# Kernel optimization log

Measured on AMD Instinct MI355X. Metric: run time of the kernel, lower is better.

Reference implementation:

```python
import jax, jax.numpy as jnp
import numpy as np

B = 32          # graphs per batch
NPG = 2048      # nodes per graph
N = B * NPG     # 65536 total nodes
EPG = 16384     # edges per graph
E = B * EPG     # 524288 total edges
F_IN = 129
H, C = 4, 64    # heads, per-head channels
HC = H * C      # 256
NEG_SLOPE = 0.2 # GATConv LeakyReLU slope


def setup_inputs() -> dict:
    key = jax.random.key(0)
    ks = jax.random.split(key, 20)
    # node features
    x = jax.random.normal(ks[0], (N, F_IN), dtype=jnp.float32)
    # random edges, endpoints within the same graph (per-graph contiguous node ids)
    off = (jnp.arange(B) * NPG)[:, None]
    src = (jax.random.randint(ks[1], (B, EPG), 0, NPG) + off).reshape(-1)
    dst = (jax.random.randint(ks[2], (B, EPG), 0, NPG) + off).reshape(-1)
    edge_index = jnp.stack([src, dst]).astype(jnp.int64)

    def lin(k, fan_in, shape):
        return jax.random.normal(k, shape, dtype=jnp.float32) / np.sqrt(fan_in)

    return {
        "x": x,
        "edge_index": edge_index,
        "lin0_w": lin(ks[3], F_IN, (F_IN, 256)),
        "lin0_b": jnp.zeros((256,), jnp.float32),
        "gat0_W": lin(ks[4], 256, (256, HC)),
        "gat0_asrc": lin(ks[5], C, (H, C)),
        "gat0_adst": lin(ks[6], C, (H, C)),
        "gat0_b": jnp.zeros((HC,), jnp.float32),
        "pool0_w": lin(ks[7], HC, (HC,)),
        "gat1_W": lin(ks[8], HC, (HC, HC)),
        "gat1_asrc": lin(ks[9], C, (H, C)),
        "gat1_adst": lin(ks[10], C, (H, C)),
        "gat1_b": jnp.zeros((HC,), jnp.float32),
        "pool1_w": lin(ks[11], HC, (HC,)),
        "gate_w": lin(ks[12], HC, (HC, 1)),
        "gate_b": jnp.zeros((1,), jnp.float32),
    }


def _leaky(z):
    return jnp.where(z > 0, z, NEG_SLOPE * z)


def _gat(h_in, src, dst, emask, W, asrc, adst, b):
    """PyG GATConv: shared lin, edge attention, segment softmax over dest, self-loops, concat heads."""
    n = h_in.shape[0]
    h = (h_in @ W).reshape(n, H, C)                       # [n,H,C]
    loops = jnp.arange(n)
    s = jnp.concatenate([src, loops])                     # add self loops
    d = jnp.concatenate([dst, loops])
    m = jnp.concatenate([emask, jnp.ones((n,), bool)])
    a_s = jnp.einsum('nhc,hc->nh', h, asrc)               # [n,H]
    a_d = jnp.einsum('nhc,hc->nh', h, adst)
    logit = _leaky(a_s[s] + a_d[d])                       # [E+n,H]
    logit = jnp.where(m[:, None], logit, -1e9)
    mx = jax.ops.segment_max(logit, d, num_segments=n)    # stable segment softmax
    ex = jnp.exp(logit - mx[d]) * m[:, None].astype(logit.dtype)
    den = jax.ops.segment_sum(ex, d, num_segments=n)
    coef = ex / (den[d] + 1e-16)                          # [E+n,H]
    out = jax.ops.segment_sum(h[s] * coef[:, :, None], d, num_segments=n)
    return out.reshape(n, HC) + b


def _topk_pool(hx, src, dst, emask, w, n_in, k):
    """PyG TopKPooling: score = x.w/||w||, per-graph top-k, x' = x[perm]*tanh(score[perm]), edge filter+reindex."""
    n_tot = hx.shape[0]
    bb = n_tot // n_in
    score = (hx @ w) / (jnp.linalg.norm(w) + 1e-16)       # [n_tot]
    _, idx = jax.lax.top_k(score.reshape(bb, n_in), k)    # [bb,k]
    perm = (idx + (jnp.arange(bb) * n_in)[:, None]).reshape(-1)
    xs = hx[perm] * jnp.tanh(score[perm])[:, None]
    newid = jnp.full((n_tot,), -1, jnp.int32).at[perm].set(jnp.arange(bb * k, dtype=jnp.int32))
    ns, nd = newid[src], newid[dst]
    valid = emask & (ns >= 0) & (nd >= 0)
    ns = jnp.where(valid, ns, 0)
    nd = jnp.where(valid, nd, 0)
    return xs, ns, nd, valid


def _attpool(hx, n, gate_w, gate_b):
    """AttentionalAggregation: softmax(gate_nn(x)) per graph, weighted sum."""
    bb = hx.shape[0] // n
    gate = (hx @ gate_w + gate_b).reshape(bb, n)
    wts = jax.nn.softmax(gate, axis=1)
    return jnp.einsum('bn,bnf->bf', wts, hx.reshape(bb, n, -1))


def reference(x, edge_index, lin0_w, lin0_b, gat0_W, gat0_asrc, gat0_adst, gat0_b,
              pool0_w, gat1_W, gat1_asrc, gat1_adst, gat1_b, pool1_w, gate_w, gate_b):
    src, dst = edge_index[0], edge_index[1]
    emask = jnp.ones((E,), bool)
    h = jax.nn.relu(x @ lin0_w + lin0_b)                                  # hidden MLP
    h = jax.nn.elu(_gat(h, src, dst, emask, gat0_W, gat0_asrc, gat0_adst, gat0_b))
    h, src, dst, emask = _topk_pool(h, src, dst, emask, pool0_w, NPG, NPG // 2)
    out = _attpool(h, NPG // 2, gate_w, gate_b)                           # [B,256]
    h = jax.nn.elu(_gat(h, src, dst, emask, gat1_W, gat1_asrc, gat1_adst, gat1_b))
    h, src, dst, emask = _topk_pool(h, src, dst, emask, pool1_w, NPG // 2, NPG // 4)
    out = out + _attpool(h, NPG // 4, gate_w, gate_b)
    return out
```

## Files before the change

kernel.cpp:

```cpp
#include <hip/hip_runtime.h>
#include <cmath>

namespace {

constexpr int NN0 = 65536;
constexpr int NB  = 32;
constexpr int NE  = 524288;
constexpr int EPG = 16384;
constexpr int FIN = 129;
constexpr int KP  = 160;

typedef short bf16x8 __attribute__((ext_vector_type(8)));
typedef float f32x4 __attribute__((ext_vector_type(4)));

__device__ inline float leakyrelu(float z) { return z > 0.f ? z : 0.2f * z; }
__device__ inline float eluf(float z) { return z > 0.f ? z : __expf(z) - 1.f; }
__device__ inline float ftanh(float z) {
  float t = __expf(2.f * z);
  return (t - 1.f) / (t + 1.f);
}

__device__ inline unsigned short f2bf(float x) {
  union { float f; unsigned int u; } v; v.f = x;
  unsigned int r = v.u + 0x7fffu + ((v.u >> 16) & 1u);
  return (unsigned short)(r >> 16);
}
__device__ inline float bf2f(unsigned short h) {
  union { unsigned int u; float f; } v; v.u = ((unsigned int)h) << 16;
  return v.f;
}

__device__ inline float4 f4fma(float4 a, float c, float4 acc) {
  acc.x += a.x * c; acc.y += a.y * c; acc.z += a.z * c; acc.w += a.w * c;
  return acc;
}

__device__ inline int swz_block(int bid, int bpgl) {
  int x = bid & 7;
  int local = bid >> 3;
  int g = x + ((local >> bpgl) << 3);
  return (g << bpgl) + (local & ((1 << bpgl) - 1));
}

__device__ __forceinline__ void gload_lds16(const unsigned short* g, unsigned short* l) {
  __builtin_amdgcn_global_load_lds((const unsigned int*)g, (unsigned int*)l, 16, 0, 0);
}

__device__ inline void pack_w_body(const float* __restrict__ W, int Kreal, int idx,
                                   unsigned short* __restrict__ hi,
                                   unsigned short* __restrict__ lo) {
  int j = idx & 7;
  int lane = (idx >> 3) & 63;
  int ct = (idx >> 9) & 15;
  int kt = idx >> 13;
  int k = kt * 32 + ((lane >> 4) << 3) + j;
  int c = ct * 16 + (lane & 15);
  float v = (k < Kreal) ? W[(size_t)k * 256 + c] : 0.f;
  unsigned short h = f2bf(v);
  hi[idx] = h;
  lo[idx] = f2bf(v - bf2f(h));
}

constexpr int SLC = 8;

__global__ __launch_bounds__(1024) void prep(
    const float* __restrict__ x,
    const float* __restrict__ w0, const float* __restrict__ w1,
    const float* __restrict__ w2,
    const float* __restrict__ pw0, const float* __restrict__ pw1,
    const int* __restrict__ src, const int* __restrict__ dst,
    unsigned short* __restrict__ xhi, unsigned short* __restrict__ xlo,
    unsigned short* __restrict__ whi0, unsigned short* __restrict__ wlo0,
    unsigned short* __restrict__ whi1, unsigned short* __restrict__ wlo1,
    unsigned short* __restrict__ whi2, unsigned short* __restrict__ wlo2,
    float* __restrict__ norms, int* __restrict__ newid,
    int* __restrict__ cursor, int* __restrict__ csr) {
  __shared__ int cnt[2048];
  __shared__ int basev[2048];
  const int NSC = NB * SLC;
  const int NX = NN0 * KP / 8192;
  const int NW0 = 5 * 8192 / 1024;
  const int NW = 8 * 8192 / 1024;
  const int NC = NN0 / 1024;
  int b = blockIdx.x, tid = threadIdx.x;
  if (b < NSC) {
    const int g = b / SLC, sl = b % SLC;
    const int e0 = g * EPG + sl * (EPG / SLC);
    const int ne = EPG / SLC;
    cnt[tid] = 0; cnt[tid + 1024] = 0;
    __syncthreads();
    for (int i = tid; i < ne; i += 1024)
      atomicAdd(&cnt[dst[e0 + i] - (g << 11)], 1);
    __syncthreads();
    for (int k = tid; k < 2048; k += 1024) {
      int c = cnt[k];
      basev[k] = c ? atomicAdd(&cursor[(g << 11) + k], c) : 0;
    }
    __syncthreads();
    cnt[tid] = 0; cnt[tid + 1024] = 0;
    __syncthreads();
    for (int i = tid; i < ne; i += 1024) {
      int e = e0 + i;
      int d = dst[e];
      int lb = d - (g << 11);
      int pos = basev[lb] + atomicAdd(&cnt[lb], 1);
      if (pos < 64) csr[(size_t)d * 64 + pos] = src[e];
    }
    return;
  }
  b -= NSC;
  if (b < NX) {
    const int base = (b * 1024 + tid) * 8;
    const int row = base / KP;
    const int c0 = base - row * KP;
    const float* xr = &x[(size_t)row * FIN];
    bf16x8 hv, lv;
#pragma unroll
    for (int i = 0; i < 8; i++) {
      const int c = c0 + i;
      float v = (c < FIN) ? xr[c] : 0.f;
      unsigned short h = f2bf(v);
      hv[i] = (short)h;
      lv[i] = (short)f2bf(v - bf2f(h));
    }
    *reinterpret_cast<bf16x8*>(&xhi[base]) = hv;
    *reinterpret_cast<bf16x8*>(&xlo[base]) = lv;
    return;
  }
  b -= NX;
  if (b < NW0) { pack_w_body(w0, FIN, b * 1024 + tid, whi0, wlo0); return; }
  b -= NW0;
  if (b < NW) { pack_w_body(w1, 256, b * 1024 + tid, whi1, wlo1); return; }
  b -= NW;
  if (b < NW) { pack_w_body(w2, 256, b * 1024 + tid, whi2, wlo2); return; }
  b -= NW;
  if (b < NC) {
    newid[b * 1024 + tid] = -1;
    return;
  }
  if (tid < 64) {
    float a0 = 0.f, a1 = 0.f;
#pragma unroll
    for (int j = tid; j < 256; j += 64) {
      float v0 = pw0[j]; a0 += v0 * v0;
      float v1 = pw1[j]; a1 += v1 * v1;
    }
#pragma unroll
    for (int off = 32; off >= 1; off >>= 1) {
      a0 += __shfl_xor(a0, off);
      a1 += __shfl_xor(a1, off);
    }
    if (tid == 0) {
      norms[0] = 1.f / (sqrtf(a0) + 1e-16f);
      norms[1] = 1.f / (sqrtf(a1) + 1e-16f);
    }
  }
}

__global__ __launch_bounds__(256, 2) void gemm_fused(
    const unsigned short* __restrict__ Xhi, const unsigned short* __restrict__ Xlo,
    const unsigned short* __restrict__ B0hi, const unsigned short* __restrict__ B0lo,
    const float* __restrict__ bias0,
    const unsigned short* __restrict__ B1hi, const unsigned short* __restrict__ B1lo,
    float* __restrict__ Out,
    const float* __restrict__ attsrc, const float* __restrict__ attdst,
    float* __restrict__ a_s, float* __restrict__ a_d) {
  __shared__ __align__(16) unsigned short As[2][2][64][32];
  __shared__ __align__(16) char Hsh[2][64 * 512];
  const int tid = threadIdx.x;
  const int lane = tid & 63;
  const int w = tid >> 6;
  const int row0 = blockIdx.x * 64;
  const int l15 = lane & 15, q = lane >> 4;
  const int srow16 = lane >> 2;
  const int skc = (lane & 3) * 8;

  auto stage = [&](int nb, int kt) {
    const size_t goff = (size_t)(row0 + w * 16 + srow16) * KP + kt * 32 + skc;
    gload_lds16(Xhi + goff, &As[nb][0][w * 16][0]);
    gload_lds16(Xlo + goff, &As[nb][1][w * 16][0]);
  };

  f32x4 acc[4][4];
#pragma unroll
  for (int mf = 0; mf < 4; mf++)
#pragma unroll
    for (int nf = 0; nf < 4; nf++) acc[mf][nf] = (f32x4)(0.f);

  stage(0, 0);
  __syncthreads();

#pragma unroll
  for (int kt = 0; kt < 5; ++kt) {
    const int nb = kt & 1;
    if (kt + 1 < 5) stage(nb ^ 1, kt + 1);
    bf16x8 bh[4], bl[4];
#pragma unroll
    for (int nf = 0; nf < 4; nf++) {
      const int ct = w * 4 + nf;
      const size_t bbase = ((size_t)((kt * 16 + ct) * 64 + lane)) << 3;
      bh[nf] = *reinterpret_cast<const bf16x8*>(B0hi + bbase);
      bl[nf] = *reinterpret_cast<const bf16x8*>(B0lo + bbase);
    }
#pragma unroll
    for (int mf = 0; mf < 4; mf++) {
      const int ar = mf * 16 + l15;
      bf16x8 ah = *reinterpret_cast<const bf16x8*>(&As[nb][0][ar][q * 8]);
      bf16x8 al = *reinterpret_cast<const bf16x8*>(&As[nb][1][ar][q * 8]);
#pragma unroll
      for (int nf = 0; nf < 4; nf++) {
        acc[mf][nf] = __builtin_amdgcn_mfma_f32_16x16x32_bf16(ah, bh[nf], acc[mf][nf], 0, 0, 0);
        acc[mf][nf] = __builtin_amdgcn_mfma_f32_16x16x32_bf16(ah, bl[nf], acc[mf][nf], 0, 0, 0);
        acc[mf][nf] = __builtin_amdgcn_mfma_f32_16x16x32_bf16(al, bh[nf], acc[mf][nf], 0, 0, 0);
      }
    }
    __syncthreads();
  }

#pragma unroll
  for (int mf = 0; mf < 4; mf++) {
#pragma unroll
    for (int r = 0; r < 4; r++) {
      const int row = mf * 16 + q * 4 + r;
#pragma unroll
      for (int nf = 0; nf < 4; nf++) {
        const int col = w * 64 + nf * 16 + l15;
        float v = acc[mf][nf][r] + bias0[col];
        v = fmaxf(v, 0.f);
        unsigned short h = f2bf(v);
        unsigned short l = f2bf(v - bf2f(h));
        unsigned int off = (unsigned int)(row * 512 + col * 2) ^ ((row & 7) << 4);
        *reinterpret_cast<unsigned short*>(&Hsh[0][off]) = h;
        *reinterpret_cast<unsigned short*>(&Hsh[1][off]) = l;
        acc[mf][nf][r] = 0.f;
      }
    }
  }
  __syncthreads();

#pragma unroll
  for (int kt = 0; kt < 8; ++kt) {
    bf16x8 bh[4], bl[4];
#pragma unroll
    for (int nf = 0; nf < 4; nf++) {
      const int ct = w * 4 + nf;
      const size_t bbase = ((size_t)((kt * 16 + ct) * 64 + lane)) << 3;
      bh[nf] = *reinterpret_cast<const bf16x8*>(B1hi + bbase);
      bl[nf] = *reinterpret_cast<const bf16x8*>(B1lo + bbase);
    }
#pragma unroll
    for (int mf = 0; mf < 4; mf++) {
      const int ar = mf * 16 + l15;
      unsigned int off = (unsigned int)(ar * 512 + kt * 64 + q * 16) ^ ((ar & 7) << 4);
      bf16x8 ah = *reinterpret_cast<const bf16x8*>(&Hsh[0][off]);
      bf16x8 al = *reinterpret_cast<const bf16x8*>(&Hsh[1][off]);
#pragma unroll
      for (int nf = 0; nf < 4; nf++) {
        acc[mf][nf] = __builtin_amdgcn_mfma_f32_16x16x32_bf16(ah, bh[nf], acc[mf][nf], 0, 0, 0);
        acc[mf][nf] = __builtin_amdgcn_mfma_f32_16x16x32_bf16(ah, bl[nf], acc[mf][nf], 0, 0, 0);
        acc[mf][nf] = __builtin_amdgcn_mfma_f32_16x16x32_bf16(al, bh[nf], acc[mf][nf], 0, 0, 0);
      }
    }
  }

#pragma unroll
  for (int mf = 0; mf < 4; mf++) {
    const int rowb = row0 + mf * 16 + q * 4;
#pragma unroll
    for (int r = 0; r < 4; r++) {
#pragma unroll
      for (int nf = 0; nf < 4; nf++) {
        const int col = w * 64 + nf * 16 + l15;
        Out[(size_t)(rowb + r) * 256 + col] = acc[mf][nf][r];
      }
    }
  }
  const int head = w;
  float sv[4], dv[4];
#pragma unroll
  for (int nf = 0; nf < 4; nf++) {
    sv[nf] = attsrc[head * 64 + nf * 16 + l15];
    dv[nf] = attdst[head * 64 + nf * 16 + l15];
  }
#pragma unroll
  for (int mf = 0; mf < 4; mf++) {
#pragma unroll
    for (int r = 0; r < 4; r++) {
      float ps = 0.f, pd = 0.f;
#pragma unroll
      for (int nf = 0; nf < 4; nf++) {
        ps += acc[mf][nf][r] * sv[nf];
        pd += acc[mf][nf][r] * dv[nf];
      }
#pragma unroll
      for (int off = 8; off >= 1; off >>= 1) {
        ps += __shfl_xor(ps, off);
        pd += __shfl_xor(pd, off);
      }
      if (l15 == 0) {
        const int row = row0 + mf * 16 + q * 4 + r;
        a_s[(size_t)row * 4 + head] = ps;
        a_d[(size_t)row * 4 + head] = pd;
      }
    }
  }
}

template <int KT, bool INDIR>
__global__ __launch_bounds__(256, 2) void gemm_mfma(
    const unsigned short* __restrict__ Xhi, const unsigned short* __restrict__ Xlo,
    int ldx,
    const unsigned short* __restrict__ Bhi, const unsigned short* __restrict__ Blo,
    float* __restrict__ Out,
    const float* __restrict__ attsrc, const float* __restrict__ attdst,
    float* __restrict__ a_s, float* __restrict__ a_d,
    const int* __restrict__ rowmap, const float* __restrict__ tscale, int swzl,
    int ngemm, const float* __restrict__ partials, float* __restrict__ outp,
    int nch) {
  __shared__ __align__(16) unsigned short As[2][2][128][32];
  const int tid = threadIdx.x;
  if ((int)blockIdx.x >= ngemm) {
    int g = blockIdx.x - ngemm, c = tid;
    float a = 0.f;
    for (int s = 0; s < nch; s++) a += partials[((size_t)g * nch + s) * 256 + c];
    outp[g * 256 + c] = a;
    return;
  }
  const int lane = tid & 63;
  const int w = tid >> 6;
  const int rb = (swzl >= 0) ? swz_block(blockIdx.x, swzl) : blockIdx.x;
  const int row0 = rb * 128;
  const int l15 = lane & 15, q = lane >> 4;
  const int sl4 = lane >> 2;
  const int skc = (lane & 3) * 8;

  size_t gr[2];
#pragma unroll
  for (int i = 0; i < 2; i++) {
    int lr = row0 + (w + 4 * i) * 16 + sl4;
    gr[i] = INDIR ? (size_t)rowmap[lr] : (size_t)lr;
  }

  auto stage = [&](int nb, int kt) {
#pragma unroll
    for (int i = 0; i < 2; i++) {
      const int rbase = (w + 4 * i) * 16;
      const size_t goff = gr[i] * ldx + kt * 32 + skc;
      gload_lds16(Xhi + goff, &As[nb][0][rbase][0]);
      gload_lds16(Xlo + goff, &As[nb][1][rbase][0]);
    }
  };

  f32x4 acc[8][4];
#pragma unroll
  for (int mf = 0; mf < 8; mf++)
#pragma unroll
    for (int nf = 0; nf < 4; nf++) acc[mf][nf] = (f32x4)(0.f);

  stage(0, 0);
  __syncthreads();

#pragma unroll
  for (int kt = 0; kt < KT; ++kt) {
    const int nb = kt & 1;
    if (kt + 1 < KT) stage(nb ^ 1, kt + 1);
    bf16x8 bh[4], bl[4];
#pragma unroll
    for (int nf = 0; nf < 4; nf++) {
      const int ct = w * 4 + nf;
      const size_t bbase = ((size_t)((kt * 16 + ct) * 64 + lane)) << 3;
      bh[nf] = *reinterpret_cast<const bf16x8*>(Bhi + bbase);
      bl[nf] = *reinterpret_cast<const bf16x8*>(Blo + bbase);
    }
#pragma unroll
    for (int mf = 0; mf < 8; mf++) {
      const int ar = mf * 16 + l15;
      bf16x8 ah = *reinterpret_cast<const bf16x8*>(&As[nb][0][ar][q * 8]);
      bf16x8 al = *reinterpret_cast<const bf16x8*>(&As[nb][1][ar][q * 8]);
#pragma unroll
      for (int nf = 0; nf < 4; nf++) {
        acc[mf][nf] = __builtin_amdgcn_mfma_f32_16x16x32_bf16(ah, bh[nf], acc[mf][nf], 0, 0, 0);
        acc[mf][nf] = __builtin_amdgcn_mfma_f32_16x16x32_bf16(ah, bl[nf], acc[mf][nf], 0, 0, 0);
        acc[mf][nf] = __builtin_amdgcn_mfma_f32_16x16x32_bf16(al, bh[nf], acc[mf][nf], 0, 0, 0);
      }
    }
    __syncthreads();
  }

#pragma unroll
  for (int mf = 0; mf < 8; mf++) {
    const int rowb = row0 + mf * 16 + q * 4;
#pragma unroll
    for (int r = 0; r < 4; r++) {
      const float ts = INDIR ? tscale[rowb + r] : 1.f;
#pragma unroll
      for (int nf = 0; nf < 4; nf++) {
        float v = acc[mf][nf][r];
        if constexpr (INDIR) v *= ts;
        const int col = w * 64 + nf * 16 + l15;
        Out[(size_t)(rowb + r) * 256 + col] = v;
      }
    }
  }
  const int head = w;
  float sv[4], dv[4];
#pragma unroll
  for (int nf = 0; nf < 4; nf++) {
    sv[nf] = attsrc[head * 64 + nf * 16 + l15];
    dv[nf] = attdst[head * 64 + nf * 16 + l15];
  }
#pragma unroll
  for (int mf = 0; mf < 8; mf++) {
#pragma unroll
    for (int r = 0; r < 4; r++) {
      float ps = 0.f, pd = 0.f;
#pragma unroll
      for (int nf = 0; nf < 4; nf++) {
        ps += acc[mf][nf][r] * sv[nf];
        pd += acc[mf][nf][r] * dv[nf];
      }
#pragma unroll
      for (int off = 8; off >= 1; off >>= 1) {
        ps += __shfl_xor(ps, off);
        pd += __shfl_xor(pd, off);
      }
      if (l15 == 0) {
        const int row = row0 + mf * 16 + q * 4 + r;
        float ts = INDIR ? tscale[row] : 1.f;
        a_s[(size_t)row * 4 + head] = ps * ts;
        a_d[(size_t)row * 4 + head] = pd * ts;
      }
    }
  }
}

__global__ __launch_bounds__(256) void gat_node8(
    const int* __restrict__ cursor, const int* __restrict__ csr,
    const float* __restrict__ a_s, const float* __restrict__ a_d,
    const float* __restrict__ hW, const float* __restrict__ bias,
    const float* __restrict__ pool_w, const float* __restrict__ inv_norm,
    const float* __restrict__ gate_w,
    unsigned short* __restrict__ outHi, unsigned short* __restrict__ outLo,
    float* __restrict__ score, float* __restrict__ graw, int bpgl) {
  const int lane = threadIdx.x & 63;
  const int wv = threadIdx.x >> 6;
  const int dbase = swz_block(blockIdx.x, bpgl) * 8 + wv * 2;
  const int g = lane >> 4, l16 = lane & 15;
  const int d = dbase + (g >> 1);
  const int h0 = (g & 1) * 2;

  const int deg = min(cursor[d], 63);
  const int dim = deg + 1;

  int dmaxw = dim;
  dmaxw = max(dmaxw, __shfl_xor(dmaxw, 32));
  const int nch = (dmaxw + 15) >> 4;

  const float2 ad2 = *reinterpret_cast<const float2*>(&a_d[(size_t)d * 4 + h0]);

  int sreg[4];
  float L0[4], L1[4];
#pragma unroll
  for (int c = 0; c < 4; c++) {
    if (c < nch) {
      const int j = c * 16 + l16;
      const bool has = j < dim;
      int s = (j < deg) ? csr[(size_t)d * 64 + j] : d;
      sreg[c] = s;
      float2 as2 = *reinterpret_cast<const float2*>(&a_s[(size_t)s * 4 + h0]);
      L0[c] = has ? leakyrelu(as2.x + ad2.x) : -1e30f;
      L1[c] = has ? leakyrelu(as2.y + ad2.y) : -1e30f;
    } else {
      sreg[c] = d;
      L0[c] = -1e30f; L1[c] = -1e30f;
    }
  }
  float m0 = fmaxf(fmaxf(L0[0], L0[1]), fmaxf(L0[2], L0[3]));
  float m1 = fmaxf(fmaxf(L1[0], L1[1]), fmaxf(L1[2], L1[3]));
#pragma unroll
  for (int off = 1; off <= 8; off <<= 1) {
    m0 = fmaxf(m0, __shfl_xor(m0, off));
    m1 = fmaxf(m1, __shfl_xor(m1, off));
  }
  float e0[4], e1[4];
  float dn0 = 0.f, dn1 = 0.f;
#pragma unroll
  for (int c = 0; c < 4; c++) {
    if (c < nch) {
      e0[c] = __expf(L0[c] - m0);
      e1[c] = __expf(L1[c] - m1);
      dn0 += e0[c]; dn1 += e1[c];
    } else {
      e0[c] = 0.f; e1[c] = 0.f;
    }
  }
#pragma unroll
  for (int off = 1; off <= 8; off <<= 1) {
    dn0 += __shfl_xor(dn0, off);
    dn1 += __shfl_xor(dn1, off);
  }

  float4 acc0 = {0.f, 0.f, 0.f, 0.f}, acc1 = {0.f, 0.f, 0.f, 0.f};
#pragma unroll
  for (int c = 0; c < 4; c++) {
    if (c < nch) {
      const int tmax = min(16, dmaxw - c * 16);
#pragma unroll 4
      for (int tt = 0; tt < tmax; tt++) {
        const int idx = g * 16 + tt;
        int st = __shfl(sreg[c], idx);
        float c0 = __shfl(e0[c], idx), c1 = __shfl(e1[c], idx);
        if (c * 16 + tt < dim) {
          const float4* hp = reinterpret_cast<const float4*>(&hW[(size_t)st * 256]) + l16;
          acc0 = f4fma(hp[h0 * 16],       c0, acc0);
          acc1 = f4fma(hp[(h0 + 1) * 16], c1, acc1);
        }
      }
    }
  }

  const float iv0 = 1.f / (dn0 + 1e-16f), iv1 = 1.f / (dn1 + 1e-16f);
  float sd = 0.f, gd = 0.f;
#pragma unroll
  for (int h = 0; h < 2; h++) {
    const int coff = (h0 + h) * 64 + l16 * 4;
    float4 vb = h ? acc1 : acc0;
    float iv = h ? iv1 : iv0;
    float4 bb = *reinterpret_cast<const float4*>(&bias[coff]);
    float4 o;
    o.x = eluf(vb.x * iv + bb.x);
    o.y = eluf(vb.y * iv + bb.y);
    o.z = eluf(vb.z * iv + bb.z);
    o.w = eluf(vb.w * iv + bb.w);
    ushort4 oh, ol;
    oh.x = f2bf(o.x); ol.x = f2bf(o.x - bf2f(oh.x));
    oh.y = f2bf(o.y); ol.y = f2bf(o.y - bf2f(oh.y));
    oh.z = f2bf(o.z); ol.z = f2bf(o.z - bf2f(oh.z));
    oh.w = f2bf(o.w); ol.w = f2bf(o.w - bf2f(oh.w));
    *reinterpret_cast<ushort4*>(&outHi[(size_t)d * 256 + coff]) = oh;
    *reinterpret_cast<ushort4*>(&outLo[(size_t)d * 256 + coff]) = ol;
    float4 pw = *reinterpret_cast<const float4*>(&pool_w[coff]);
    float4 gw = *reinterpret_cast<const float4*>(&gate_w[coff]);
    sd += o.x * pw.x + o.y * pw.y + o.z * pw.z + o.w * pw.w;
    gd += o.x * gw.x + o.y * gw.y + o.z * gw.z + o.w * gw.w;
  }
#pragma unroll
  for (int off = 1; off <= 16; off <<= 1) {
    sd += __shfl_xor(sd, off);
    gd += __shfl_xor(gd, off);
  }
  if ((lane & 31) == 0) {
    score[d] = sd * inv_norm[0];
    graw[d] = gd;
  }
}

__global__ __launch_bounds__(1024) void topk_hsel(
    const float* __restrict__ score, const float* __restrict__ graw,
    const float* __restrict__ gate_b, int npg, int k,
    int* __restrict__ perm, int* __restrict__ newid,
    float* __restrict__ gate, float* __restrict__ tsc) {
  __shared__ unsigned keys[2048];
  __shared__ int hist[1024];
  __shared__ int ssum[1024];
  __shared__ int segtot[16];
  __shared__ unsigned wmin[16], wmax[16];
  __shared__ int sstate[3];
  __shared__ int scnt;
  __shared__ int candi[512];
  __shared__ unsigned candk[512];
  __shared__ float fred[1024];
  const int g = blockIdx.x, tid = threadIdx.x;
  const int wv = tid >> 6, ln = tid & 63;
  const size_t base = (size_t)g * npg;

  unsigned mymin = 0xFFFFFFFFu, mymax = 0u;
  for (int i = tid; i < npg; i += 1024) {
    unsigned u = __float_as_uint(score[base + i]);
    u = (u & 0x80000000u) ? ~u : (u | 0x80000000u);
    keys[i] = u;
    mymin = min(mymin, u);
    mymax = max(mymax, u);
  }
#pragma unroll
  for (int off = 32; off >= 1; off >>= 1) {
    mymin = min(mymin, (unsigned)__shfl_xor((int)mymin, off));
    mymax = max(mymax, (unsigned)__shfl_xor((int)mymax, off));
  }
  if (ln == 0) { wmin[wv] = mymin; wmax[wv] = mymax; }
  __syncthreads();
  unsigned lo, hi;
  {
    unsigned a = 0xFFFFFFFFu, b = 0u;
#pragma unroll
    for (int i = 0; i < 16; i++) { a = min(a, wmin[i]); b = max(b, wmax[i]); }
    lo = a; hi = b;
  }
  int need = k;

  for (int iter = 0; iter < 4; ++iter) {
    unsigned long long range = (unsigned long long)(hi - lo) + 1ull;
    unsigned width = (unsigned)((range + 1023ull) >> 10);
    hist[tid] = 0;
    __syncthreads();
    for (int i = tid; i < npg; i += 1024) {
      unsigned u = keys[i];
      if (u >= lo && u <= hi) atomicAdd(&hist[(u - lo) / width], 1);
    }
    __syncthreads();
    int v = hist[tid];
    int s = v;
#pragma unroll
    for (int off = 1; off < 64; off <<= 1) {
      int t = __shfl_down(s, off);
      if (ln + off < 64) s += t;
    }
    if (ln == 0) segtot[wv] = s;
    __syncthreads();
    if (tid == 0) {
      int acc = 0;
      for (int i = 15; i >= 0; i--) { int t = segtot[i]; segtot[i] = acc; acc += t; }
    }
    __syncthreads();
    int S = s + segtot[wv];
    ssum[tid] = S;
    __syncthreads();
    int gt = (tid == 1023) ? 0 : ssum[tid + 1];
    if (S >= need && gt < need) {
      sstate[0] = tid;
      sstate[1] = gt;
      sstate[2] = hist[tid];
    }
    __syncthreads();
    const int bstar = sstate[0], cntAbove = sstate[1], m = sstate[2];
    unsigned nlo = lo + (unsigned)bstar * width;
    unsigned long long nhiu = (unsigned long long)lo + (unsigned long long)(bstar + 1) * width - 1ull;
    unsigned nhi = (nhiu > (unsigned long long)hi) ? hi : (unsigned)nhiu;
    need -= cntAbove;
    lo = nlo; hi = nhi;
    __syncthreads();
    if (width == 1 || m <= 256) break;
  }

  if (tid == 0) scnt = 0;
  __syncthreads();
  for (int i = tid; i < npg; i += 1024) {
    unsigned u = keys[i];
    if (u >= lo && u <= hi) {
      int pidx = atomicAdd(&scnt, 1);
      if (pidx < 512) { candi[pidx] = i; candk[pidx] = u; }
    }
  }
  __syncthreads();
  const int m_all = scnt;
  const float gb = gate_b[0];
  if (tid == 0) scnt = 0;
  __syncthreads();
  for (int i = tid; i < npg; i += 1024) {
    if (keys[i] > hi) {
      int pos = atomicAdd(&scnt, 1);
      int node = (int)(base + i);
      perm[g * k + pos] = node;
      if (newid) newid[node] = g * k + pos;
      float ts = ftanh(score[base + i]);
      tsc[g * k + pos] = ts;
      gate[g * k + pos] = ts * graw[node] + gb;
    }
  }
  __syncthreads();
  const int nAbove = scnt;
  if (m_all <= 512) {
    for (int c = tid; c < m_all; c += 1024) {
      unsigned u = candk[c];
      int i = candi[c];
      int rank = 0;
      for (int j = 0; j < m_all; j++) {
        unsigned vk = candk[j];
        rank += (vk > u) || (vk == u && candi[j] < i);
      }
      if (rank < need) {
        int pos = nAbove + rank;
        int node = (int)(base + i);
        perm[g * k + pos] = node;
        if (newid) newid[node] = g * k + pos;
        float ts = ftanh(score[base + i]);
        tsc[g * k + pos] = ts;
        gate[g * k + pos] = ts * graw[node] + gb;
      }
    }
  } else {
    for (int i = tid; i < npg; i += 1024) {
      unsigned u = keys[i];
      if (u >= lo && u <= hi) {
        int rank = 0;
        for (int j = 0; j < npg; j++) {
          unsigned vk = keys[j];
          if (vk >= lo && vk <= hi) rank += (vk > u) || (vk == u && j < i);
        }
        if (rank < need) {
          int pos = nAbove + rank;
          int node = (int)(base + i);
          perm[g * k + pos] = node;
          if (newid) newid[node] = g * k + pos;
          float ts = ftanh(score[base + i]);
          tsc[g * k + pos] = ts;
          gate[g * k + pos] = ts * graw[node] + gb;
        }
      }
    }
  }
  __syncthreads();

  float gv = (tid < k) ? gate[g * k + tid] : -1e30f;
  fred[tid] = gv;
  __syncthreads();
  for (int s = 512; s >= 1; s >>= 1) {
    if (tid < s) fred[tid] = fmaxf(fred[tid], fred[tid + s]);
    __syncthreads();
  }
  const float gm = fred[0];
  __syncthreads();
  float ge = (tid < k) ? __expf(gv - gm) : 0.f;
  fred[tid] = ge;
  __syncthreads();
  for (int s = 512; s >= 1; s >>= 1) {
    if (tid < s) fred[tid] += fred[tid + s];
    __syncthreads();
  }
  const float ginv = 1.f / fred[0];
  if (tid < k) gate[g * k + tid] = ge * ginv * tsc[g * k + tid];
}

__global__ __launch_bounds__(1024) void pool_tail(
    const unsigned short* __restrict__ xhi, const unsigned short* __restrict__ xlo,
    const int* __restrict__ perm, const float* __restrict__ wfin,
    float* __restrict__ partials, int npg, int bpgl, int nsc,
    const int* __restrict__ src, const int* __restrict__ dst,
    const int* __restrict__ newid, int* __restrict__ cursor2,
    int* __restrict__ csr) {
  __shared__ int cnt[1024];
  __shared__ int basev[1024];
  const int tid = threadIdx.x;
  if ((int)blockIdx.x < nsc) {
    const int g = blockIdx.x / SLC, sl = blockIdx.x % SLC;
    const int e0 = g * EPG + sl * (EPG / SLC);
    const int ne = EPG / SLC;
    cnt[tid] = 0;
    __syncthreads();
    for (int i = tid; i < ne; i += 1024) {
      int e = e0 + i;
      int s = newid[src[e]], d = newid[dst[e]];
      if (s >= 0 && d >= 0) atomicAdd(&cnt[d - (g << 10)], 1);
    }
    __syncthreads();
    {
      int c = cnt[tid];
      basev[tid] = c ? atomicAdd(&cursor2[(g << 10) + tid], c) : 0;
    }
    __syncthreads();
    cnt[tid] = 0;
    __syncthreads();
    for (int i = tid; i < ne; i += 1024) {
      int e = e0 + i;
      int s = newid[src[e]], d = newid[dst[e]];
      if (s < 0 || d < 0) continue;
      int lb = d - (g << 10);
      int pos = basev[lb] + atomicAdd(&cnt[lb], 1);
      if (pos < 64) csr[(size_t)d * 64 + pos] = s;
    }
    return;
  }
  int rel = blockIdx.x - nsc;
  int o = swz_block(rel, bpgl);
  int g = o >> bpgl, lb = o & ((1 << bpgl) - 1);
  int part = tid >> 8, c = tid & 255;
  int sub = lb * 4 + part;
  size_t r0 = (size_t)g * npg + sub * 32;
  float a = 0.f;
#pragma unroll 8
  for (int i = 0; i < 32; i++) {
    float wv = wfin[r0 + i];
    size_t node = (size_t)perm[r0 + i];
    float v = bf2f(xhi[node * 256 + c]) + bf2f(xlo[node * 256 + c]);
    a += wv * v;
  }
  partials[((size_t)g * (npg >> 5) + sub) * 256 + c] = a;
}

__global__ __launch_bounds__(256) void attpool_reduce(const float* __restrict__ partials,
                                                      float* __restrict__ out,
                                                      int nch, int acc_flag) {
  int g = blockIdx.x, c = threadIdx.x;
  float a = 0.f;
  for (int s = 0; s < nch; s++) a += partials[((size_t)g * nch + s) * 256 + c];
  if (acc_flag) out[g * 256 + c] += a;
  else out[g * 256 + c] = a;
}

}

extern "C" void kernel_launch(void* const* d_in, const int* in_sizes, int n_in,
                              void* d_out, int out_size, void* d_ws, size_t ws_size,
                              hipStream_t stream) {
  (void)in_sizes; (void)n_in; (void)out_size; (void)ws_size;
  const float* x       = (const float*)d_in[0];
  const int*   ei      = (const int*)d_in[1];
  const float* lin0_w  = (const float*)d_in[2];
  const float* lin0_b  = (const float*)d_in[3];
  const float* gat0_W  = (const float*)d_in[4];
  const float* gat0_as = (const float*)d_in[5];
  const float* gat0_ad = (const float*)d_in[6];
  const float* gat0_b  = (const float*)d_in[7];
  const float* pool0_w = (const float*)d_in[8];
  const float* gat1_W  = (const float*)d_in[9];
  const float* gat1_as = (const float*)d_in[10];
  const float* gat1_ad = (const float*)d_in[11];
  const float* gat1_b  = (const float*)d_in[12];
  const float* pool1_w = (const float*)d_in[13];
  const float* gate_w  = (const float*)d_in[14];
  const float* gate_b  = (const float*)d_in[15];
  float* out = (float*)d_out;
  const int* srcp = ei;
  const int* dstp = ei + NE;

  char* wsb = (char*)d_ws;
  size_t cur = 0;
  auto alloc = [&](size_t bytes) {
    void* p = wsb + cur;
    cur = (cur + bytes + 255) & ~(size_t)255;
    return p;
  };
  char* regA = (char*)alloc((size_t)NN0 * 256 * 4);
  char* regB = (char*)alloc((size_t)NN0 * 256 * 4);
  char* regD = (char*)alloc((size_t)NN0 * KP * 2 * 2);
  float* a_s     = (float*)alloc((size_t)NN0 * 4 * 4);
  float* a_d     = (float*)alloc((size_t)NN0 * 4 * 4);
  int*   cursor  = (int*)alloc((size_t)NN0 * 4);
  int*   cursor2 = (int*)alloc((size_t)32768 * 4);
  int*   csr     = (int*)alloc((size_t)NN0 * 64 * 4);
  float* score   = (float*)alloc((size_t)NN0 * 4);
  float* graw    = (float*)alloc((size_t)NN0 * 4);
  int*   newid   = (int*)alloc((size_t)NN0 * 4);
  int*   perm0   = (int*)alloc((size_t)32768 * 4);
  int*   perm1   = (int*)alloc((size_t)16384 * 4);
  float* tsc0    = (float*)alloc((size_t)32768 * 4);
  float* tsc1    = (float*)alloc((size_t)16384 * 4);
  float* gate0   = (float*)alloc((size_t)32768 * 4);
  float* gate1   = (float*)alloc((size_t)16384 * 4);
  float* partials= (float*)alloc((size_t)NB * 32 * 256 * 4);
  float* norms   = (float*)alloc(2 * 4);
  unsigned short* whi0 = (unsigned short*)alloc((size_t)5 * 8192 * 2);
  unsigned short* wlo0 = (unsigned short*)alloc((size_t)5 * 8192 * 2);
  unsigned short* whi1 = (unsigned short*)alloc((size_t)8 * 8192 * 2);
  unsigned short* wlo1 = (unsigned short*)alloc((size_t)8 * 8192 * 2);
  unsigned short* whi2 = (unsigned short*)alloc((size_t)8 * 8192 * 2);
  unsigned short* wlo2 = (unsigned short*)alloc((size_t)8 * 8192 * 2);

  unsigned short* xhi = (unsigned short*)regD;
  unsigned short* xlo = xhi + (size_t)NN0 * KP;
  float* hW0  = (float*)regB;
  unsigned short* out0hi = (unsigned short*)regA;
  unsigned short* out0lo = out0hi + (size_t)NN0 * 256;
  float* hW1  = (float*)regB;
  unsigned short* out1hi = (unsigned short*)(regB + (size_t)32768 * 256 * 4);
  unsigned short* out1lo = out1hi + (size_t)32768 * 256;

  hipMemsetAsync(cursor, 0, (size_t)NN0 * 4, stream);
  hipMemsetAsync(cursor2, 0, (size_t)32768 * 4, stream);

  {
    int grid = NB * SLC + NN0 * KP / 8192 + 40 + 64 + 64 + 64 + 1;
    prep<<<grid, 1024, 0, stream>>>(x, lin0_w, gat0_W, gat1_W, pool0_w, pool1_w,
                                    srcp, dstp,
                                    xhi, xlo, whi0, wlo0, whi1, wlo1, whi2, wlo2,
                                    norms, newid, cursor, csr);
  }

  gemm_fused<<<NN0 / 64, 256, 0, stream>>>(
      xhi, xlo, whi0, wlo0, lin0_b, whi1, wlo1, hW0,
      gat0_as, gat0_ad, a_s, a_d);

  gat_node8<<<NN0 / 8, 256, 0, stream>>>(cursor, csr, a_s, a_d, hW0,
                                         gat0_b, pool0_w, norms, gate_w,
                                         out0hi, out0lo, score, graw, 8);

  topk_hsel<<<NB, 1024, 0, stream>>>(score, graw, gate_b, 2048, 1024,
                                     perm0, newid, gate0, tsc0);
  pool_tail<<<NB * SLC + NB * 8, 1024, 0, stream>>>(
      out0hi, out0lo, perm0, gate0, partials, 1024, 3, NB * SLC,
      srcp, dstp, newid, cursor2, csr);

  gemm_mfma<8, true><<<32768 / 128 + NB, 256, 0, stream>>>(
      out0hi, out0lo, 256, whi2, wlo2, hW1,
      gat1_as, gat1_ad, a_s, a_d, perm0, tsc0, 3,
      32768 / 128, partials, out, 32);

  gat_node8<<<32768 / 8, 256, 0, stream>>>(cursor2, csr, a_s, a_d, hW1,
                                           gat1_b, pool1_w, norms + 1, gate_w,
                                           out1hi, out1lo, score, graw, 7);

  topk_hsel<<<NB, 1024, 0, stream>>>(score, graw, gate_b, 1024, 512,
                                     perm1, nullptr, gate1, tsc1);
  pool_tail<<<NB * 4, 1024, 0, stream>>>(
      out1hi, out1lo, perm1, gate1, partials, 512, 2, 0,
      nullptr, nullptr, nullptr, nullptr, nullptr);
  attpool_reduce<<<NB, 256, 0, stream>>>(partials, out, 16, 1);
}
```

Measured before the change: 249.3 us.

## Halve intermediate LDS buffer in fused GEMM by staging second GEMM in two K halves

The fused two-GEMM kernel now keeps the ReLU'd first-GEMM output packed as bf16 hi/lo pairs in registers. It writes only half of the K dimension to shared memory at a time: waves 0-1 write, everyone runs four K-steps, then waves 2-3 write and the rest runs. This halves the Hsh LDS buffer and raises launch bounds to 3 blocks per CU to increase occupancy. In exchange it adds two extra block barriers and 64 packed registers per thread, which may cause spills under the tighter register budget.

```diff
diff --git a/kernel.cpp b/kernel.cpp
--- a/kernel.cpp
+++ b/kernel.cpp
@@ -157,7 +157,7 @@
   }
 }
 
-__global__ __launch_bounds__(256, 2) void gemm_fused(
+__global__ __launch_bounds__(256, 3) void gemm_fused(
     const unsigned short* __restrict__ Xhi, const unsigned short* __restrict__ Xlo,
     const unsigned short* __restrict__ B0hi, const unsigned short* __restrict__ B0lo,
     const float* __restrict__ bias0,
@@ -166,7 +166,7 @@
     const float* __restrict__ attsrc, const float* __restrict__ attdst,
     float* __restrict__ a_s, float* __restrict__ a_d) {
   __shared__ __align__(16) unsigned short As[2][2][64][32];
-  __shared__ __align__(16) char Hsh[2][64 * 512];
+  __shared__ __align__(16) char Hsh[2][64 * 256];
   const int tid = threadIdx.x;
   const int lane = tid & 63;
   const int w = tid >> 6;
@@ -217,51 +217,87 @@
     __syncthreads();
   }
 
+  unsigned hp[32], lp[32];
 #pragma unroll
   for (int mf = 0; mf < 4; mf++) {
 #pragma unroll
-    for (int r = 0; r < 4; r++) {
-      const int row = mf * 16 + q * 4 + r;
+    for (int nf = 0; nf < 4; nf++) {
+      const int col = w * 64 + nf * 16 + l15;
+      const float bb = bias0[col];
+#pragma unroll
+      for (int rp = 0; rp < 2; rp++) {
+        float v0 = fmaxf(acc[mf][nf][2 * rp] + bb, 0.f);
+        float v1 = fmaxf(acc[mf][nf][2 * rp + 1] + bb, 0.f);
+        unsigned short h0 = f2bf(v0);
+        unsigned short l0 = f2bf(v0 - bf2f(h0));
+        unsigned short h1 = f2bf(v1);
+        unsigned short l1 = f2bf(v1 - bf2f(h1));
+        const int i = mf * 8 + nf * 2 + rp;
+        hp[i] = (unsigned)h0 | ((unsigned)h1 << 16);
+        lp[i] = (unsigned)l0 | ((unsigned)l1 << 16);
+        acc[mf][nf][2 * rp] = 0.f;
+        acc[mf][nf][2 * rp + 1] = 0.f;
+      }
+    }
+  }
+
+  auto writeHalf = [&]() {
+#pragma unroll
+    for (int mf = 0; mf < 4; mf++) {
 #pragma unroll
       for (int nf = 0; nf < 4; nf++) {
-        const int col = w * 64 + nf * 16 + l15;
-        float v = acc[mf][nf][r] + bias0[col];
-        v = fmaxf(v, 0.f);
-        unsigned short h = f2bf(v);
-        unsigned short l = f2bf(v - bf2f(h));
-        unsigned int off = (unsigned int)(row * 512 + col * 2) ^ ((row & 7) << 4);
-        *reinterpret_cast<unsigned short*>(&Hsh[0][off]) = h;
-        *reinterpret_cast<unsigned short*>(&Hsh[1][off]) = l;
-        acc[mf][nf][r] = 0.f;
-      }
-    }
-  }
-  __syncthreads();
-
-#pragma unroll
-  for (int kt = 0; kt < 8; ++kt) {
-    bf16x8 bh[4], bl[4];
-#pragma unroll
-    for (int nf = 0; nf < 4; nf++) {
-      const int ct = w * 4 + nf;
-      const size_t bbase = ((size_t)((kt * 16 + ct) * 64 + lane)) << 3;
-      bh[nf] = *reinterpret_cast<const bf16x8*>(B1hi + bbase);
-      bl[nf] = *reinterpret_cast<const bf16x8*>(B1lo + bbase);
-    }
-#pragma unroll
-    for (int mf = 0; mf < 4; mf++) {
-      const int ar = mf * 16 + l15;
-      unsigned int off = (unsigned int)(ar * 512 + kt * 64 + q * 16) ^ ((ar & 7) << 4);
-      bf16x8 ah = *reinterpret_cast<const bf16x8*>(&Hsh[0][off]);
-      bf16x8 al = *reinterpret_cast<const bf16x8*>(&Hsh[1][off]);
+#pragma unroll
+        for (int r = 0; r < 4; r++) {
+          const int i = mf * 8 + nf * 2 + (r >> 1);
+          unsigned short pv = (r & 1) ? (unsigned short)(hp[i] >> 16)
+                                      : (unsigned short)(hp[i] & 0xffffu);
+          unsigned short pl = (r & 1) ? (unsigned short)(lp[i] >> 16)
+                                      : (unsigned short)(lp[i] & 0xffffu);
+          const int row = mf * 16 + q * 4 + r;
+          const int colL = (w & 1) * 64 + nf * 16 + l15;
+          unsigned off = (unsigned)(row * 256 + colL * 2) ^ ((row & 7) << 4);
+          *reinterpret_cast<unsigned short*>(&Hsh[0][off]) = pv;
+          *reinterpret_cast<unsigned short*>(&Hsh[1][off]) = pl;
+        }
+      }
+    }
+  };
+
+  auto mfma4 = [&](int ktbase) {
+#pragma unroll
+    for (int ktp = 0; ktp < 4; ++ktp) {
+      const int kt = ktbase + ktp;
+      bf16x8 bh[4], bl[4];
 #pragma unroll
       for (int nf = 0; nf < 4; nf++) {
-        acc[mf][nf] = __builtin_amdgcn_mfma_f32_16x16x32_bf16(ah, bh[nf], acc[mf][nf], 0, 0, 0);
-        acc[mf][nf] = __builtin_amdgcn_mfma_f32_16x16x32_bf16(ah, bl[nf], acc[mf][nf], 0, 0, 0);
-        acc[mf][nf] = __builtin_amdgcn_mfma_f32_16x16x32_bf16(al, bh[nf], acc[mf][nf], 0, 0, 0);
-      }
-    }
-  }
+        const int ct = w * 4 + nf;
+        const size_t bbase = ((size_t)((kt * 16 + ct) * 64 + lane)) << 3;
+        bh[nf] = *reinterpret_cast<const bf16x8*>(B1hi + bbase);
+        bl[nf] = *reinterpret_cast<const bf16x8*>(B1lo + bbase);
+      }
+#pragma unroll
+      for (int mf = 0; mf < 4; mf++) {
+        const int ar = mf * 16 + l15;
+        unsigned off = (unsigned)(ar * 256 + (ktp * 32 + q * 8) * 2) ^ ((ar & 7) << 4);
+        bf16x8 ah = *reinterpret_cast<const bf16x8*>(&Hsh[0][off]);
+        bf16x8 al = *reinterpret_cast<const bf16x8*>(&Hsh[1][off]);
+#pragma unroll
+        for (int nf = 0; nf < 4; nf++) {
+          acc[mf][nf] = __builtin_amdgcn_mfma_f32_16x16x32_bf16(ah, bh[nf], acc[mf][nf], 0, 0, 0);
+          acc[mf][nf] = __builtin_amdgcn_mfma_f32_16x16x32_bf16(ah, bl[nf], acc[mf][nf], 0, 0, 0);
+          acc[mf][nf] = __builtin_amdgcn_mfma_f32_16x16x32_bf16(al, bh[nf], acc[mf][nf], 0, 0, 0);
+        }
+      }
+    }
+  };
+
+  if (w < 2) writeHalf();
+  __syncthreads();
+  mfma4(0);
+  __syncthreads();
+  if (w >= 2) writeHalf();
+  __syncthreads();
+  mfma4(4);
 
 #pragma unroll
   for (int mf = 0; mf < 4; mf++) {
```

Result: slower. 407.4 us (+63.4%).
